# Performance work log

Hardware: AMD Instinct MI355X
Metric: run time of the kernel (lower is better)

## Reference

```python
import jax, jax.numpy as jnp
import numpy as np

N = 100000      # nodes
E = 1600000     # edges (before self-loops)
IN = 64         # in_channels
HID = 16        # hidden_channels
HEADS = 4       # num_heads
G = 512         # number of graphs in batch
SLOPE = 0.2     # GATConv leaky_relu negative_slope


def setup_inputs() -> dict:
    key = jax.random.key(0)
    ks = jax.random.split(key, 12)
    s = 0.1
    x = jax.random.normal(ks[0], (N, IN), jnp.float32)
    edge_index = jax.random.randint(ks[1], (2, E), 0, N, dtype=jnp.int64)
    batch = jnp.sort(jax.random.randint(ks[2], (N,), 0, G, dtype=jnp.int64))
    W1 = jax.random.normal(ks[3], (IN, HEADS * HID), jnp.float32) * s
    a1_src = jax.random.normal(ks[4], (HEADS, HID), jnp.float32) * s
    a1_dst = jax.random.normal(ks[5], (HEADS, HID), jnp.float32) * s
    b1 = jnp.zeros((HEADS * HID,), jnp.float32)
    W2 = jax.random.normal(ks[6], (HEADS * HID, HID), jnp.float32) * s
    a2_src = jax.random.normal(ks[7], (1, HID), jnp.float32) * s
    a2_dst = jax.random.normal(ks[8], (1, HID), jnp.float32) * s
    b2 = jnp.zeros((HID,), jnp.float32)
    Wc = jax.random.normal(ks[9], (HID, 1), jnp.float32) * s
    bc = jnp.zeros((1,), jnp.float32)
    return dict(x=x, edge_index=edge_index, batch=batch, W1=W1, a1_src=a1_src,
                a1_dst=a1_dst, b1=b1, W2=W2, a2_src=a2_src, a2_dst=a2_dst,
                b2=b2, Wc=Wc, bc=bc)


def gat_layer(x, src, dst, W, a_s, a_d, bias, heads, out_ch, concat):
    # PyG GATConv: linear -> per-edge attention logits -> segment softmax over dst -> scatter aggregate
    n = x.shape[0]
    h = (x @ W).reshape(n, heads, out_ch)              # [N, H, C]
    al_s = jnp.sum(h * a_s, axis=-1)                   # [N, H]
    al_d = jnp.sum(h * a_d, axis=-1)                   # [N, H]
    e = al_s[src] + al_d[dst]                          # [E, H]
    e = jnp.where(e > 0, e, SLOPE * e)                 # leaky_relu
    m = jax.ops.segment_max(e, dst, num_segments=n)    # per-dst max (self-loops ensure non-empty)
    p = jnp.exp(e - m[dst])
    denom = jax.ops.segment_sum(p, dst, num_segments=n)
    alpha = p / (denom[dst] + 1e-16)                   # [E, H]
    out = jax.ops.segment_sum(h[src] * alpha[:, :, None], dst, num_segments=n)  # [N, H, C]
    out = out.reshape(n, heads * out_ch) if concat else out.mean(axis=1)
    return out + bias


def reference(x, edge_index, batch, W1, a1_src, a1_dst, b1, W2, a2_src, a2_dst, b2, Wc, bc):
    loops = jnp.arange(N, dtype=edge_index.dtype)      # GATConv add_self_loops=True
    src = jnp.concatenate([edge_index[0], loops])
    dst = jnp.concatenate([edge_index[1], loops])
    h = jax.nn.elu(gat_layer(x, src, dst, W1, a1_src, a1_dst, b1, HEADS, HID, True))
    # dropout inactive (eval mode)
    h = jax.nn.elu(gat_layer(h, src, dst, W2, a2_src, a2_dst, b2, 1, HID, False))
    counts = jax.ops.segment_sum(jnp.ones((N,), h.dtype), batch, num_segments=G)
    pooled = jax.ops.segment_sum(h, batch, num_segments=G) / jnp.maximum(counts, 1.0)[:, None]
    return pooled @ Wc + bc
```

## Files before the change

kernel.cpp:

```cpp
#include <hip/hip_runtime.h>
#include <hip/hip_fp16.h>
#include <hip/hip_fp8.h>

#define N_NODES 100000
#define N_EDGES 1600000
#define ET      (N_EDGES + N_NODES)
#define NG      512
#define SLOPE   0.2f

#define BKT_SHIFT 9
#define NB_B   ((N_NODES + 511) / 512)
#define CHUNK_A 8192
#define NBLK_A ((ET + CHUNK_A - 1) / CHUNK_A)
#define H1B    ((N_NODES + 255) / 256)

typedef _Float16 half8_t __attribute__((ext_vector_type(8)));
typedef float    f32x4_t __attribute__((ext_vector_type(4)));

__global__ __launch_bounds__(256) void k_prep(
    const float* __restrict__ x, const float* __restrict__ W1,
    const float* __restrict__ a1s, const float* __restrict__ a1d,
    const int* __restrict__ ei,
    __hip_fp8_e4m3* __restrict__ h1, float* __restrict__ al1s, float* __restrict__ al1d,
    int* __restrict__ bsize)
{
    __shared__ float Wl[64 * 64];
    __shared__ float asf[64], adf[64];
    __shared__ int hcnt[NB_B];
    int tid = threadIdx.x;

    if (blockIdx.x >= H1B) {
        for (int i = tid; i < NB_B; i += 256) hcnt[i] = 0;
        __syncthreads();
        int base = (blockIdx.x - H1B) * CHUNK_A;
        int m = min(CHUNK_A, ET - base);
        for (int i = tid; i < m; i += 256) {
            int eid = base + i;
            int d = (eid < N_EDGES) ? ei[N_EDGES + eid] : (eid - N_EDGES);
            atomicAdd(&hcnt[d >> BKT_SHIFT], 1);
        }
        __syncthreads();
        for (int i = tid; i < NB_B; i += 256)
            if (hcnt[i]) atomicAdd(&bsize[i], hcnt[i]);
        return;
    }

    for (int i = tid; i < 64 * 64; i += 256) Wl[i] = W1[i];
    if (tid < 64) { asf[tid] = a1s[tid]; adf[tid] = a1d[tid]; }
    __syncthreads();

    int wv = tid >> 6, lane = tid & 63;
    int m = lane & 15, q = lane >> 4;

    half8_t bf[4][2];
#pragma unroll
    for (int t = 0; t < 4; ++t)
#pragma unroll
        for (int s = 0; s < 2; ++s) {
            half8_t b;
#pragma unroll
            for (int j = 0; j < 8; ++j)
                b[j] = (_Float16)Wl[(s * 32 + q * 8 + j) * 64 + t * 16 + m];
            bf[t][s] = b;
        }

    for (int it = 0; it < 4; ++it) {
        int node0 = blockIdx.x * 256 + wv * 64 + it * 16;
        int node = node0 + m;
        half8_t av0 = {}, av1 = {};
        if (node < N_NODES) {
            const float4* xr = (const float4*)(x + (long long)node * 64);
            float4 p0 = xr[q * 2], p1 = xr[q * 2 + 1];
            float4 p2 = xr[q * 2 + 8], p3 = xr[q * 2 + 9];
            av0[0] = (_Float16)p0.x; av0[1] = (_Float16)p0.y;
            av0[2] = (_Float16)p0.z; av0[3] = (_Float16)p0.w;
            av0[4] = (_Float16)p1.x; av0[5] = (_Float16)p1.y;
            av0[6] = (_Float16)p1.z; av0[7] = (_Float16)p1.w;
            av1[0] = (_Float16)p2.x; av1[1] = (_Float16)p2.y;
            av1[2] = (_Float16)p2.z; av1[3] = (_Float16)p2.w;
            av1[4] = (_Float16)p3.x; av1[5] = (_Float16)p3.y;
            av1[6] = (_Float16)p3.z; av1[7] = (_Float16)p3.w;
        }
        f32x4_t acc[4] = {{0,0,0,0},{0,0,0,0},{0,0,0,0},{0,0,0,0}};
#pragma unroll
        for (int t = 0; t < 4; ++t) {
            acc[t] = __builtin_amdgcn_mfma_f32_16x16x32_f16(av0, bf[t][0], acc[t], 0, 0, 0);
            acc[t] = __builtin_amdgcn_mfma_f32_16x16x32_f16(av1, bf[t][1], acc[t], 0, 0, 0);
        }
#pragma unroll
        for (int r = 0; r < 4; ++r) {
            int nr = node0 + q * 4 + r;
            bool ok = nr < N_NODES;
#pragma unroll
            for (int t = 0; t < 4; ++t) {
                float v = acc[t][r];
                if (ok) h1[(long long)nr * 64 + t * 16 + m] = __hip_fp8_e4m3(v);
                float ps = v * asf[t * 16 + m];
                float pd = v * adf[t * 16 + m];
                ps += __shfl_xor(ps, 1); ps += __shfl_xor(ps, 2);
                ps += __shfl_xor(ps, 4); ps += __shfl_xor(ps, 8);
                pd += __shfl_xor(pd, 1); pd += __shfl_xor(pd, 2);
                pd += __shfl_xor(pd, 4); pd += __shfl_xor(pd, 8);
                if (ok && m == t) { al1s[nr * 4 + t] = ps; al1d[nr * 4 + t] = pd; }
            }
        }
    }
}

__global__ __launch_bounds__(256) void k_scanB(const int* __restrict__ bsize,
                                               int* __restrict__ bbase, int* __restrict__ bcur)
{
    __shared__ int tmp[256];
    int tid = threadIdx.x;
    int v = (tid < NB_B) ? bsize[tid] : 0;
    tmp[tid] = v;
    __syncthreads();
    for (int off = 1; off < 256; off <<= 1) {
        int t = (tid >= off) ? tmp[tid - off] : 0;
        __syncthreads();
        tmp[tid] += t;
        __syncthreads();
    }
    if (tid < NB_B) { int e = tmp[tid] - v; bbase[tid] = e; bcur[tid] = e; }
}

__global__ __launch_bounds__(1024) void k_passA(const int* __restrict__ ei,
                                                int* __restrict__ bcur, unsigned int* __restrict__ ebuf)
{
    __shared__ unsigned int stage[CHUNK_A];
    __shared__ unsigned char sbin[CHUNK_A];
    __shared__ int hist[NB_B];
    __shared__ int binst[NB_B];
    __shared__ int resv[NB_B];
    __shared__ int cur[NB_B];
    __shared__ int tmp[1024];
    int tid = threadIdx.x;
    int base = blockIdx.x * CHUNK_A;
    int m = min(CHUNK_A, ET - base);
    for (int i = tid; i < NB_B; i += 1024) hist[i] = 0;
    __syncthreads();
    for (int i = tid; i < m; i += 1024) {
        int eid = base + i;
        int d = (eid < N_EDGES) ? ei[N_EDGES + eid] : (eid - N_EDGES);
        atomicAdd(&hist[d >> BKT_SHIFT], 1);
    }
    __syncthreads();
    int v = (tid < NB_B) ? hist[tid] : 0;
    tmp[tid] = v;
    __syncthreads();
    for (int off = 1; off < 1024; off <<= 1) {
        int t = (tid >= off) ? tmp[tid - off] : 0;
        __syncthreads();
        tmp[tid] += t;
        __syncthreads();
    }
    if (tid < NB_B) {
        int e = tmp[tid] - v;
        binst[tid] = e;
        cur[tid] = e;
        resv[tid] = v ? atomicAdd(&bcur[tid], v) : 0;
    }
    __syncthreads();
    for (int i = tid; i < m; i += 1024) {
        int eid = base + i;
        int s, d;
        if (eid < N_EDGES) { s = ei[eid]; d = ei[N_EDGES + eid]; }
        else               { s = eid - N_EDGES; d = s; }
        int b = d >> BKT_SHIFT;
        int pos = atomicAdd(&cur[b], 1);
        stage[pos] = ((unsigned int)(d & 511) << 17) | (unsigned int)s;
        sbin[pos] = (unsigned char)b;
    }
    __syncthreads();
    for (int i = tid; i < m; i += 1024) {
        int b = sbin[i];
        ebuf[resv[b] + (i - binst[b])] = stage[i];
    }
}

__global__ __launch_bounds__(1024) void k_passB(
    const unsigned int* __restrict__ ebuf, const int* __restrict__ bbase,
    const int* __restrict__ bsize,
    int* __restrict__ csr, int* __restrict__ offs, int* __restrict__ deg)
{
    __shared__ int ldeg[512];
    __shared__ int lofs[512];
    __shared__ int lcur[512];
    int tid = threadIdx.x;
    int b = blockIdx.x;
    int nb0 = b << BKT_SHIFT;
    int nn = min(512, N_NODES - nb0);
    int gbase = bbase[b], cnt = bsize[b];
    if (tid < 512) ldeg[tid] = 0;
    __syncthreads();
    for (int i = tid; i < cnt; i += 1024)
        atomicAdd(&ldeg[ebuf[gbase + i] >> 17], 1);
    __syncthreads();
    int v = 0;
    if (tid < 512) { v = ldeg[tid]; lofs[tid] = v; }
    __syncthreads();
    for (int off = 1; off < 512; off <<= 1) {
        int t = (tid >= off && tid < 512) ? lofs[tid - off] : 0;
        __syncthreads();
        if (tid < 512) lofs[tid] += t;
        __syncthreads();
    }
    if (tid < 512) {
        int e = lofs[tid] - v;
        lcur[tid] = e;
        if (tid < nn) { offs[nb0 + tid] = gbase + e; deg[nb0 + tid] = v; }
    }
    __syncthreads();
    for (int i = tid; i < cnt; i += 1024) {
        unsigned int ev = ebuf[gbase + i];
        int dl = ev >> 17, s = (int)(ev & 0x1FFFF);
        int p = atomicAdd(&lcur[dl], 1);
        csr[gbase + p] = s;
    }
}

__global__ __launch_bounds__(256) void k_agg1(
    const int* __restrict__ offs, const int* __restrict__ deg, const int* __restrict__ csr,
    const __hip_fp8_e4m3* __restrict__ h1, const float* __restrict__ al1s, const float* __restrict__ al1d,
    const float* __restrict__ b1, const float* __restrict__ W2,
    const float* __restrict__ a2s, const float* __restrict__ a2d,
    __half* __restrict__ h2, float* __restrict__ al2s, float* __restrict__ al2d)
{
    __shared__ float W2l[64 * 16];
    __shared__ float2 swarr[4][4][64];
    __shared__ float h1b[4][64];
    __shared__ float h2s[4][16];
    int tid = threadIdx.x;
    for (int i = tid; i < 64 * 16; i += 256) W2l[i] = W2[i];
    __syncthreads();

    int wv = tid >> 6, lane = tid & 63;
    int c = lane, h = lane >> 4;
    int node = blockIdx.x * 4 + wv;
    int st = offs[node], dg = deg[node];
    const float4 ald4 = *(const float4*)(al1d + node * 4);

    float acc = 0.f, den = 0.f;
    for (int base = 0; base < dg; base += 64) {
        int m = min(64, dg - base);
        if (lane < m) {
            int s = csr[st + base + lane];
            const float4 as4 = *(const float4*)(al1s + s * 4);
            float e0 = as4.x + ald4.x; e0 = e0 > 0.f ? e0 : SLOPE * e0;
            float e1 = as4.y + ald4.y; e1 = e1 > 0.f ? e1 : SLOPE * e1;
            float e2 = as4.z + ald4.z; e2 = e2 > 0.f ? e2 : SLOPE * e2;
            float e3 = as4.w + ald4.w; e3 = e3 > 0.f ? e3 : SLOPE * e3;
            float sx = __int_as_float(s << 6);
            swarr[wv][0][lane] = make_float2(sx, __expf(e0));
            swarr[wv][1][lane] = make_float2(sx, __expf(e1));
            swarr[wv][2][lane] = make_float2(sx, __expf(e2));
            swarr[wv][3][lane] = make_float2(sx, __expf(e3));
        }
#pragma unroll 4
        for (int j = 0; j < m; ++j) {
            float2 sw = swarr[wv][h][j];
            int s64 = __float_as_int(sw.x);
            float wgt = sw.y;
            acc = fmaf(wgt, (float)h1[s64 + c], acc);
            den += wgt;
        }
    }
    float v = acc / (den + 1e-16f) + b1[c];
    v = v > 0.f ? v : expm1f(v);
    h1b[wv][c] = v;
    if (c < 16) {
        float a = 0.f;
#pragma unroll
        for (int k = 0; k < 64; ++k) a = fmaf(h1b[wv][k], W2l[k * 16 + c], a);
        h2[node * 16 + c] = __float2half_rn(a);
        h2s[wv][c] = a;
    }
    if (c == 0) {
        float s2 = 0.f, d2 = 0.f;
#pragma unroll
        for (int j = 0; j < 16; ++j) {
            float v2 = h2s[wv][j];
            s2 = fmaf(v2, a2s[j], s2);
            d2 = fmaf(v2, a2d[j], d2);
        }
        al2s[node] = s2;
        al2d[node] = d2;
    }
}

__global__ __launch_bounds__(256) void k_agg2(
    const int* __restrict__ offs, const int* __restrict__ deg, const int* __restrict__ csr,
    const __half* __restrict__ h2, const float* __restrict__ al2s, const float* __restrict__ al2d,
    const float* __restrict__ b2, float* __restrict__ hout)
{
    __shared__ int   sarr[4][64];
    __shared__ float warr[4][64];
    int tid = threadIdx.x;
    int wv = tid >> 6, lane = tid & 63;
    int ec = lane >> 3, cc = lane & 7;
    int node = blockIdx.x * 4 + wv;
    int st = offs[node], dg = deg[node];
    float ald = al2d[node];
    const __half2* __restrict__ h2v = (const __half2*)h2;

    float a0 = 0.f, a1 = 0.f, den = 0.f;
    for (int base = 0; base < dg; base += 64) {
        int m = min(64, dg - base);
        int s = 0; float wl = 0.f;
        if (lane < m) {
            s = csr[st + base + lane];
            float e = al2s[s] + ald;
            e = e > 0.f ? e : SLOPE * e;
            wl = __expf(e);
        }
        sarr[wv][lane] = s;
        warr[wv][lane] = wl;
        float t = wl;
#pragma unroll
        for (int x = 1; x < 64; x <<= 1) t += __shfl_xor(t, x);
        den += t;
        int m8 = (m + 7) & ~7;
#pragma unroll 2
        for (int j0 = 0; j0 < m8; j0 += 8) {
            int j = j0 + ec;
            int s2i = sarr[wv][j];
            float wgt = warr[wv][j];
            __half2 hv = h2v[s2i * 8 + cc];
            a0 = fmaf(__low2float(hv), wgt, a0);
            a1 = fmaf(__high2float(hv), wgt, a1);
        }
    }
    a0 += __shfl_xor(a0, 8);  a1 += __shfl_xor(a1, 8);
    a0 += __shfl_xor(a0, 16); a1 += __shfl_xor(a1, 16);
    a0 += __shfl_xor(a0, 32); a1 += __shfl_xor(a1, 32);
    if (lane < 8) {
        float inv = 1.f / (den + 1e-16f);
        float v0 = a0 * inv + b2[2 * cc];
        float v1 = a1 * inv + b2[2 * cc + 1];
        v0 = v0 > 0.f ? v0 : expm1f(v0);
        v1 = v1 > 0.f ? v1 : expm1f(v1);
        ((float2*)hout)[node * 8 + cc] = make_float2(v0, v1);
    }
}

__global__ __launch_bounds__(256) void k_pool(
    const float* __restrict__ hout, const int* __restrict__ batch,
    const float* __restrict__ Wc, const float* __restrict__ bc, float* __restrict__ out)
{
    __shared__ float red[16][17];
    __shared__ int bnd[2];
    int g = blockIdx.x;
    int t = threadIdx.x, c = t & 15, slot = t >> 4;
    if (t < 2) {
        int key = g + t;
        int lo = 0, hi = N_NODES;
        while (lo < hi) { int mid = (lo + hi) >> 1; if (batch[mid] < key) lo = mid + 1; else hi = mid; }
        bnd[t] = lo;
    }
    __syncthreads();
    int s = bnd[0], e = bnd[1];
    float sum = 0.f;
    for (int n = s + slot; n < e; n += 16)
        sum += hout[n * 16 + c];
    red[slot][c] = sum;
    __syncthreads();
    if (t < 16) {
        float tot = 0.f;
#pragma unroll
        for (int k = 0; k < 16; ++k) tot += red[k][t];
        float cnt = fmaxf((float)(e - s), 1.0f);
        float pc = (tot / cnt) * Wc[t];
        pc += __shfl_xor(pc, 1); pc += __shfl_xor(pc, 2);
        pc += __shfl_xor(pc, 4); pc += __shfl_xor(pc, 8);
        if (t == 0) out[g] = pc + bc[0];
    }
}

extern "C" void kernel_launch(void* const* d_in, const int* in_sizes, int n_in,
                              void* d_out, int out_size, void* d_ws, size_t ws_size,
                              hipStream_t stream)
{
    const float* x    = (const float*)d_in[0];
    const int*   ei   = (const int*)d_in[1];
    const int*   batc = (const int*)d_in[2];
    const float* W1   = (const float*)d_in[3];
    const float* a1s  = (const float*)d_in[4];
    const float* a1d  = (const float*)d_in[5];
    const float* b1   = (const float*)d_in[6];
    const float* W2   = (const float*)d_in[7];
    const float* a2s  = (const float*)d_in[8];
    const float* a2d  = (const float*)d_in[9];
    const float* b2   = (const float*)d_in[10];
    const float* Wc   = (const float*)d_in[11];
    const float* bc   = (const float*)d_in[12];
    float* out = (float*)d_out;

    char* ws = (char*)d_ws;
    size_t off = 0;
    auto carveB = [&](size_t bytes) {
        void* p = ws + off;
        off += ((bytes + 15) & ~(size_t)15);
        return p;
    };
    auto carve = [&](size_t elems) { return carveB(elems * 4); };
    int*   bsize  = (int*)  carve(NB_B);
    size_t zero_bytes = off;
    int*   bbase  = (int*)  carve(NB_B);
    int*   bcur   = (int*)  carve(NB_B);
    unsigned int* ebuf = (unsigned int*)carve(ET);
    int*   csr    = (int*)  carve(ET);
    int*   offs   = (int*)  carve(N_NODES);
    int*   deg    = (int*)  carve(N_NODES);
    __hip_fp8_e4m3* h1 = (__hip_fp8_e4m3*)carveB((size_t)N_NODES * 64);
    float* al1s   = (float*)carve((size_t)N_NODES * 4);
    float* al1d   = (float*)carve((size_t)N_NODES * 4);
    __half* h2    = (__half*)carveB((size_t)N_NODES * 16 * 2);
    float* al2s   = (float*)carve(N_NODES);
    float* al2d   = (float*)carve(N_NODES);
    float* hout   = (float*)carve((size_t)N_NODES * 16);

    hipMemsetAsync(d_ws, 0, zero_bytes, stream);

    k_prep <<<H1B + NBLK_A, 256, 0, stream>>>(x, W1, a1s, a1d, ei, h1, al1s, al1d, bsize);
    k_scanB<<<1, 256, 0, stream>>>(bsize, bbase, bcur);
    k_passA<<<NBLK_A, 1024, 0, stream>>>(ei, bcur, ebuf);
    k_passB<<<NB_B, 1024, 0, stream>>>(ebuf, bbase, bsize, csr, offs, deg);
    k_agg1 <<<N_NODES / 4, 256, 0, stream>>>(offs, deg, csr, h1, al1s, al1d,
                                             b1, W2, a2s, a2d, h2, al2s, al2d);
    k_agg2 <<<N_NODES / 4, 256, 0, stream>>>(offs, deg, csr, h2, al2s, al2d,
                                             b2, hout);
    k_pool <<<NG, 256, 0, stream>>>(hout, batc, Wc, bc, out);
}
```

Before: 291.1 us.

## Gather four fp8 channels per lane and process four edges per wave step

Restructures the layer-1 aggregation so each lane loads a packed 4-byte group of fp8 channels and the wave handles four edges at once (16 lanes per edge). Partial sums are then combined across the edge slots with cross-lane shuffles. This replaces the per-byte gathers with wider loads and cuts the serial edge-loop trip count by four. In exchange it adds shuffle reductions, pads the edge count to a multiple of four using zero weights, and changes the LDS layout to separate index and weight arrays.

New measurement: 295.3 us. Within noise of the previous version (+1.5%).

```diff
diff --git a/kernel.cpp b/kernel.cpp
--- a/kernel.cpp
+++ b/kernel.cpp
@@ -227,7 +227,8 @@
     __half* __restrict__ h2, float* __restrict__ al2s, float* __restrict__ al2d)
 {
     __shared__ float W2l[64 * 16];
-    __shared__ float2 swarr[4][4][64];
+    __shared__ int   sarr[4][64];
+    __shared__ float warr[4][4 * 72];
     __shared__ float h1b[4][64];
     __shared__ float h2s[4][16];
     int tid = threadIdx.x;
@@ -235,47 +236,70 @@
     __syncthreads();
 
     int wv = tid >> 6, lane = tid & 63;
-    int c = lane, h = lane >> 4;
+    int eslot = lane >> 4;
+    int cq = lane & 15;
+    int h = cq >> 2;
+    int cq4 = cq * 4;
     int node = blockIdx.x * 4 + wv;
     int st = offs[node], dg = deg[node];
     const float4 ald4 = *(const float4*)(al1d + node * 4);
-
-    float acc = 0.f, den = 0.f;
+    const char* __restrict__ h1c = (const char*)h1;
+
+    float a0 = 0.f, a1 = 0.f, a2 = 0.f, a3 = 0.f, den = 0.f;
     for (int base = 0; base < dg; base += 64) {
         int m = min(64, dg - base);
+        int s = 0;
+        float w0 = 0.f, w1 = 0.f, w2 = 0.f, w3 = 0.f;
         if (lane < m) {
-            int s = csr[st + base + lane];
+            s = csr[st + base + lane];
             const float4 as4 = *(const float4*)(al1s + s * 4);
             float e0 = as4.x + ald4.x; e0 = e0 > 0.f ? e0 : SLOPE * e0;
             float e1 = as4.y + ald4.y; e1 = e1 > 0.f ? e1 : SLOPE * e1;
             float e2 = as4.z + ald4.z; e2 = e2 > 0.f ? e2 : SLOPE * e2;
             float e3 = as4.w + ald4.w; e3 = e3 > 0.f ? e3 : SLOPE * e3;
-            float sx = __int_as_float(s << 6);
-            swarr[wv][0][lane] = make_float2(sx, __expf(e0));
-            swarr[wv][1][lane] = make_float2(sx, __expf(e1));
-            swarr[wv][2][lane] = make_float2(sx, __expf(e2));
-            swarr[wv][3][lane] = make_float2(sx, __expf(e3));
-        }
+            w0 = __expf(e0); w1 = __expf(e1); w2 = __expf(e2); w3 = __expf(e3);
+        }
+        sarr[wv][lane] = s << 6;
+        warr[wv][0 * 72 + lane] = w0;
+        warr[wv][1 * 72 + lane] = w1;
+        warr[wv][2 * 72 + lane] = w2;
+        warr[wv][3 * 72 + lane] = w3;
+        int m4 = (m + 3) & ~3;
 #pragma unroll 4
-        for (int j = 0; j < m; ++j) {
-            float2 sw = swarr[wv][h][j];
-            int s64 = __float_as_int(sw.x);
-            float wgt = sw.y;
-            acc = fmaf(wgt, (float)h1[s64 + c], acc);
+        for (int j0 = 0; j0 < m4; j0 += 4) {
+            int j = j0 + eslot;
+            int off = sarr[wv][j] + cq4;
+            float wgt = warr[wv][h * 72 + j];
+            unsigned int pk = *(const unsigned int*)(h1c + off);
+            a0 = fmaf(wgt, __builtin_amdgcn_cvt_f32_fp8(pk, 0), a0);
+            a1 = fmaf(wgt, __builtin_amdgcn_cvt_f32_fp8(pk, 1), a1);
+            a2 = fmaf(wgt, __builtin_amdgcn_cvt_f32_fp8(pk, 2), a2);
+            a3 = fmaf(wgt, __builtin_amdgcn_cvt_f32_fp8(pk, 3), a3);
             den += wgt;
         }
     }
-    float v = acc / (den + 1e-16f) + b1[c];
-    v = v > 0.f ? v : expm1f(v);
-    h1b[wv][c] = v;
-    if (c < 16) {
+    a0 += __shfl_xor(a0, 16); a0 += __shfl_xor(a0, 32);
+    a1 += __shfl_xor(a1, 16); a1 += __shfl_xor(a1, 32);
+    a2 += __shfl_xor(a2, 16); a2 += __shfl_xor(a2, 32);
+    a3 += __shfl_xor(a3, 16); a3 += __shfl_xor(a3, 32);
+    den += __shfl_xor(den, 16); den += __shfl_xor(den, 32);
+    if (lane < 16) {
+        float inv = 1.f / (den + 1e-16f);
+        float v0 = a0 * inv + b1[cq4 + 0]; v0 = v0 > 0.f ? v0 : expm1f(v0);
+        float v1 = a1 * inv + b1[cq4 + 1]; v1 = v1 > 0.f ? v1 : expm1f(v1);
+        float v2 = a2 * inv + b1[cq4 + 2]; v2 = v2 > 0.f ? v2 : expm1f(v2);
+        float v3 = a3 * inv + b1[cq4 + 3]; v3 = v3 > 0.f ? v3 : expm1f(v3);
+        h1b[wv][cq4 + 0] = v0; h1b[wv][cq4 + 1] = v1;
+        h1b[wv][cq4 + 2] = v2; h1b[wv][cq4 + 3] = v3;
+    }
+    if (lane < 16) {
         float a = 0.f;
 #pragma unroll
-        for (int k = 0; k < 64; ++k) a = fmaf(h1b[wv][k], W2l[k * 16 + c], a);
-        h2[node * 16 + c] = __float2half_rn(a);
-        h2s[wv][c] = a;
-    }
-    if (c == 0) {
+        for (int k = 0; k < 64; ++k) a = fmaf(h1b[wv][k], W2l[k * 16 + lane], a);
+        h2[node * 16 + lane] = __float2half_rn(a);
+        h2s[wv][lane] = a;
+    }
+    if (lane == 0) {
         float s2 = 0.f, d2 = 0.f;
 #pragma unroll
         for (int j = 0; j < 16; ++j) {
```
